# Performance work log

Hardware: AMD Instinct MI355X
Metric: run time of the kernel (lower is better)

## Reference

```python
import jax, jax.numpy as jnp
import numpy as np

B, T_ENC, FEAT, H, W2V, T_DEC, V = 32, 80, 4096, 256, 256, 30, 32000


def lstm_cell(x, h, c, w_ih, w_hh, b_ih, b_hh):
    # PyTorch LSTMCell: gates order i, f, g, o
    g = x @ w_ih.T + h @ w_hh.T + b_ih + b_hh
    i, f, gg, o = jnp.split(g, 4, axis=-1)
    c_new = jax.nn.sigmoid(f) * c + jax.nn.sigmoid(i) * jnp.tanh(gg)
    h_new = jax.nn.sigmoid(o) * jnp.tanh(c_new)
    return h_new, c_new


def setup_inputs() -> dict:
    key = jax.random.key(0)
    ks = jax.random.split(key, 13)
    s = 0.05
    return {
        'feat': jax.random.normal(ks[0], (B, T_ENC, FEAT), jnp.float32),
        'caption': jax.random.normal(ks[1], (B, T_DEC, W2V), jnp.float32),
        'caption_one_hot': jax.random.normal(ks[2], (B, T_DEC, V), jnp.float32),
        'keep_rate': 1,
        'w_ih1': jax.random.normal(ks[3], (4 * H, FEAT), jnp.float32) * s,
        'w_hh1': jax.random.normal(ks[4], (4 * H, H), jnp.float32) * s,
        'b_ih1': jax.random.normal(ks[5], (4 * H,), jnp.float32) * s,
        'b_hh1': jax.random.normal(ks[6], (4 * H,), jnp.float32) * s,
        'w_ih2': jax.random.normal(ks[7], (4 * H, H + W2V), jnp.float32) * s,
        'w_hh2': jax.random.normal(ks[8], (4 * H, H), jnp.float32) * s,
        'b_ih2': jax.random.normal(ks[9], (4 * H,), jnp.float32) * s,
        'b_hh2': jax.random.normal(ks[10], (4 * H,), jnp.float32) * s,
        'w_out': jax.random.normal(ks[11], (V, H), jnp.float32) * s,
        'b_out': jax.random.normal(ks[12], (V,), jnp.float32) * s,
    }


def reference(feat, caption, caption_one_hot, keep_rate,
              w_ih1, w_hh1, b_ih1, b_hh1,
              w_ih2, w_hh2, b_ih2, b_hh2,
              w_out, b_out):
    zeros_h = jnp.zeros((B, H), feat.dtype)
    pad1 = jnp.zeros((B, FEAT), feat.dtype)

    # ---------------- encoder: 80 steps ----------------
    def enc_step(carry, x_t):
        h1, c1, h2, c2 = carry
        h1, c1 = lstm_cell(x_t, h1, c1, w_ih1, w_hh1, b_ih1, b_hh1)
        h2, c2 = lstm_cell(jnp.concatenate([zeros_h, h1], axis=1), h2, c2,
                           w_ih2, w_hh2, b_ih2, b_hh2)
        return (h1, c1, h2, c2), h2

    (h1, c1, h2, c2), enc_h2 = jax.lax.scan(
        enc_step, (zeros_h, zeros_h, zeros_h, zeros_h),
        jnp.transpose(feat, (1, 0, 2)))
    enc_h2 = jnp.transpose(enc_h2, (1, 0, 2))  # [B, 80, H]

    # ---------------- decoder: teacher forcing (coin>=100 never fires) ----
    targets = jnp.argmax(caption_one_hot, axis=-1)  # [B, T_DEC]

    def dec_step(carry, xs):
        h1, c1, h2, c2, loss = carry
        word_t, tgt_t = xs  # [B, W2V], [B]
        h1, c1 = lstm_cell(pad1, h1, c1, w_ih1, w_hh1, b_ih1, b_hh1)
        h2n, c2 = lstm_cell(jnp.concatenate([word_t, h1], axis=1), h2, c2,
                            w_ih2, w_hh2, b_ih2, b_hh2)
        logits = h2n @ w_out.T + b_out  # [B, V]
        logp = jax.nn.log_softmax(logits, axis=-1)
        ce = -jnp.take_along_axis(logp, tgt_t[:, None], axis=1)[:, 0]
        loss = loss + jnp.mean(ce) / B  # sum(mean-CE)/batch, per original
        # attention: scores of encoder h2 states against current h2
        attn = jax.nn.softmax(jnp.einsum('bsh,bh->bs', enc_h2, h2n), axis=-1)
        ctx = jnp.einsum('bs,bsh->bh', attn, enc_h2)  # replaces h2 for next step
        return (h1, c1, ctx, c2, loss), None

    xs = (jnp.transpose(caption[:, :T_DEC - 1, :], (1, 0, 2)),
          jnp.transpose(targets[:, 1:T_DEC], (1, 0)))
    (h1, c1, h2, c2, total_loss), _ = jax.lax.scan(
        dec_step, (h1, c1, h2, c2, jnp.float32(0.0)), xs)
    return total_loss
```

## Files before the change

kernel.cpp:

```cpp
#include <hip/hip_runtime.h>
#include <hip/hip_bf16.h>
#include <math.h>

#define BB 32
#define TE 80
#define FEAT 4096
#define HH 256
#define W2V 256
#define TD 30
#define VV 32000
#define G4 1024

typedef unsigned short u16;
typedef unsigned int u32;
using f32x4 = __attribute__((ext_vector_type(4))) float;
using bf16x8 = __attribute__((ext_vector_type(8))) short;
using f16x2 = __attribute__((ext_vector_type(2))) _Float16;

#define SENT 0xFFFFFFFFu
#define GUARD (1 << 22)

__device__ __forceinline__ float sigm(float x) { return 1.0f / (1.0f + expf(-x)); }
__device__ __forceinline__ u16 f2bf(float f) {
  u32 u = __float_as_uint(f);
  u32 r = (u + 0x7FFFu + ((u >> 16) & 1u)) >> 16;
  return (u16)r;
}
__device__ __forceinline__ u32 packh2(float lo, float hi) {
  f16x2 v = {(_Float16)lo, (_Float16)hi};
  return __builtin_bit_cast(u32, v);
}

#define AT_LOAD(p)     __hip_atomic_load((p), __ATOMIC_RELAXED, __HIP_MEMORY_SCOPE_AGENT)
#define AT_STORE(p, v) __hip_atomic_store((p), (v), __ATOMIC_RELAXED, __HIP_MEMORY_SCOPE_AGENT)

__device__ __forceinline__ float fdot2h(f16x2 a, f16x2 b, float c) {
#if __has_builtin(__builtin_amdgcn_fdot2)
  return __builtin_amdgcn_fdot2(a, b, c, false);
#else
  return c + (float)a[0] * (float)b[0] + (float)a[1] * (float)b[1];
#endif
}

__global__ __launch_bounds__(256) void prep_kernel(
    const float* __restrict__ w_ih1, const float* __restrict__ w_ih2,
    const float* __restrict__ caption, const float* __restrict__ onehot,
    const float* __restrict__ b_ih1, const float* __restrict__ b_hh1,
    const float* __restrict__ b_ih2, const float* __restrict__ b_hh2,
    u16* __restrict__ w_ih1b, float* __restrict__ XW2,
    float* __restrict__ bias1, float* __restrict__ bias2,
    u32* __restrict__ H1H, u32* __restrict__ H2H, u32* __restrict__ A2P,
    float* __restrict__ loss, int* __restrict__ ctrs,
    int* __restrict__ targets) {
  __shared__ __align__(16) char psm[50688];
  int blk = blockIdx.x, tid = threadIdx.x;
  if (blk < 928) {
    int k = blk;
    int s = (k >> 5) + 1, b = k & 31;
    const float* row = &onehot[((size_t)b * TD + s) * VV];
    float bv = -INFINITY;
    int bi = 0x7fffffff;
    for (int v = tid; v < VV; v += 256) {
      float x = row[v];
      if (x > bv || (x == bv && v < bi)) { bv = x; bi = v; }
    }
    float* sv = (float*)psm;
    int* si = (int*)(psm + 1024);
    sv[tid] = bv; si[tid] = bi;
    __syncthreads();
    for (int off = 128; off; off >>= 1) {
      if (tid < off) {
        float ov = sv[tid + off]; int oi = si[tid + off];
        if (ov > sv[tid] || (ov == sv[tid] && oi < si[tid])) { sv[tid] = ov; si[tid] = oi; }
      }
      __syncthreads();
    }
    if (tid == 0) targets[k] = si[0];
  } else if (blk < 1952) {
    int i0 = (blk - 928) * 1024 + tid;
#pragma unroll
    for (int ii = 0; ii < 4; ++ii) {
      int i = i0 + ii * 256;
      float4 v = *(const float4*)&w_ih1[(size_t)i * 4];
      *(ushort4*)&w_ih1b[(size_t)i * 4] =
          make_ushort4(f2bf(v.x), f2bf(v.y), f2bf(v.z), f2bf(v.w));
    }
  } else if (blk < 2416) {
    int k = blk - 1952, nb = k & 15, t = k >> 4;
    u16* As = (u16*)psm;
    u16* Bs = (u16*)(psm + 16896);
    int nBase = nb * 64;
#pragma unroll
    for (int it = 0; it < 4; ++it) {
      int i = it * 256 + tid;
      int r = i >> 5, c8 = i & 31;
      const float* src = &caption[((size_t)r * TD + t) * 256 + c8 * 8];
      float4 v0 = *(const float4*)src;
      float4 v1 = *(const float4*)(src + 4);
      u16* dst = &As[r * 264 + c8 * 8];
      *(ushort4*)dst = make_ushort4(f2bf(v0.x), f2bf(v0.y), f2bf(v0.z), f2bf(v0.w));
      *(ushort4*)(dst + 4) = make_ushort4(f2bf(v1.x), f2bf(v1.y), f2bf(v1.z), f2bf(v1.w));
    }
#pragma unroll
    for (int it = 0; it < 8; ++it) {
      int i = it * 256 + tid;
      int r = i >> 5, c8 = i & 31;
      const float* src = &w_ih2[(size_t)(nBase + r) * 512 + c8 * 8];
      float4 v0 = *(const float4*)src;
      float4 v1 = *(const float4*)(src + 4);
      u16* dst = &Bs[r * 264 + c8 * 8];
      *(ushort4*)dst = make_ushort4(f2bf(v0.x), f2bf(v0.y), f2bf(v0.z), f2bf(v0.w));
      *(ushort4*)(dst + 4) = make_ushort4(f2bf(v1.x), f2bf(v1.y), f2bf(v1.z), f2bf(v1.w));
    }
    __syncthreads();
    int lane = tid & 63, w = tid >> 6;
    int lrow = lane & 15, lk = (lane >> 4) * 8;
    f32x4 acc[2];
    acc[0] = (f32x4){0.f, 0.f, 0.f, 0.f};
    acc[1] = (f32x4){0.f, 0.f, 0.f, 0.f};
#pragma unroll
    for (int ks = 0; ks < 8; ++ks) {
      bf16x8 bfr = *(const bf16x8*)&Bs[(w * 16 + lrow) * 264 + ks * 32 + lk];
#pragma unroll
      for (int m = 0; m < 2; ++m) {
        bf16x8 af = *(const bf16x8*)&As[(m * 16 + lrow) * 264 + ks * 32 + lk];
        acc[m] = __builtin_amdgcn_mfma_f32_16x16x32_bf16(af, bfr, acc[m], 0, 0, 0);
      }
    }
    int col = nBase + w * 16 + (lane & 15);
    float bv = b_ih2[col] + b_hh2[col];
    int orow = (lane >> 4) * 4;
#pragma unroll
    for (int m = 0; m < 2; ++m)
#pragma unroll
      for (int qq = 0; qq < 4; ++qq) {
        int bb = m * 16 + orow + qq;
        XW2[((size_t)t * 32 + bb) * G4 + col] = acc[m][qq] + bv;
      }
  } else if (blk < 2856) {
    int i = (blk - 2416) * 256 + tid;
    uint4 z = {0u, 0u, 0u, 0u};
    uint4 s = {SENT, SENT, SENT, SENT};
    uint4 v = (i < 1024) ? z : s;
    ((uint4*)H1H)[i] = v;
    ((uint4*)H2H)[i] = v;
  } else if (blk < 3296) {
    int i0 = (blk - 2856) * 1024 + tid;
    uint4 s = {SENT, SENT, SENT, SENT};
#pragma unroll
    for (int ii = 0; ii < 4; ++ii) ((uint4*)A2P)[i0 + ii * 256] = s;
  } else {
    for (int i = tid; i < 1024; i += 256) {
      bias1[i] = b_ih1[i] + b_hh1[i];
      bias2[i] = b_ih2[i] + b_hh2[i];
    }
    if (tid < 256) ctrs[tid] = 0;
    if (tid == 0) *loss = 0.0f;
  }
}

#define GBM 128
#define GBN 128
#define GBK 64
#define LDSTR 72

__global__ __launch_bounds__(256) void gemm_x1_kernel(
    const float* __restrict__ A, const u16* __restrict__ Bw,
    const float* __restrict__ bias, float* __restrict__ C) {
  __shared__ __align__(16) u16 As[GBM * LDSTR];
  __shared__ __align__(16) u16 Bs[GBN * LDSTR];
  int tid = threadIdx.x;
  int rBase = (blockIdx.x >> 3) * GBM;
  int nBase = (blockIdx.x & 7) * GBN;
  int lane = tid & 63, w = tid >> 6;
  int wrow = (w >> 1) * 64, wcol = (w & 1) * 64;
  int lrow = lane & 15, lk = (lane >> 4) * 8;

  f32x4 acc[4][4];
#pragma unroll
  for (int m = 0; m < 4; ++m)
#pragma unroll
    for (int n = 0; n < 4; ++n) acc[m][n] = (f32x4){0.f, 0.f, 0.f, 0.f};

  for (int k0 = 0; k0 < FEAT; k0 += GBK) {
#pragma unroll
    for (int i = 0; i < 8; ++i) {
      int f = i * 256 + tid;
      int r = f >> 4, c = (f & 15) << 2;
      float4 v = *(const float4*)&A[(size_t)(rBase + r) * FEAT + k0 + c];
      *(ushort4*)&As[r * LDSTR + c] =
          make_ushort4(f2bf(v.x), f2bf(v.y), f2bf(v.z), f2bf(v.w));
    }
#pragma unroll
    for (int i = 0; i < 4; ++i) {
      int f = i * 256 + tid;
      int r = f >> 3, c8 = f & 7;
      *(uint4*)&Bs[r * LDSTR + c8 * 8] =
          *(const uint4*)&Bw[(size_t)(nBase + r) * FEAT + k0 + c8 * 8];
    }
    __syncthreads();
#pragma unroll
    for (int s2 = 0; s2 < 2; ++s2) {
      bf16x8 af[4], bfr[4];
#pragma unroll
      for (int m = 0; m < 4; ++m)
        af[m] = *(const bf16x8*)&As[(wrow + m * 16 + lrow) * LDSTR + s2 * 32 + lk];
#pragma unroll
      for (int n = 0; n < 4; ++n)
        bfr[n] = *(const bf16x8*)&Bs[(wcol + n * 16 + lrow) * LDSTR + s2 * 32 + lk];
#pragma unroll
      for (int m = 0; m < 4; ++m)
#pragma unroll
        for (int n = 0; n < 4; ++n)
          acc[m][n] = __builtin_amdgcn_mfma_f32_16x16x32_bf16(
              af[m], bfr[n], acc[m][n], 0, 0, 0);
    }
    __syncthreads();
  }
  int orow = (lane >> 4) * 4;
  int ocol = lane & 15;
#pragma unroll
  for (int m = 0; m < 4; ++m)
#pragma unroll
    for (int n = 0; n < 4; ++n) {
      int cidx = nBase + wcol + n * 16 + ocol;
      float bv = bias[cidx];
#pragma unroll
      for (int q = 0; q < 4; ++q) {
        int r = rBase + wrow + m * 16 + orow + q;
        C[(size_t)r * G4 + cidx] = acc[m][n][q] + bv;
      }
    }
}

struct RP {
  const float *X1, *XW2, *bias1, *bias2;
  const float *w_hh1, *w_ih2, *w_hh2;
  u32* H1H;
  u32* H2H;
  u32* A2P;
  u16* H2NB;
};

__global__ __launch_bounds__(512, 1) void recurrent_kernel(RP p) {
  __shared__ float encL[TE][257];
  __shared__ __align__(16) f16x2 hS[128];
  __shared__ float tmp2[256];
  __shared__ float gb[256];
  __shared__ float a2pS[256];
  __shared__ float hnew[64];
  __shared__ float sc[80];
  __shared__ float red[4];
  int bid = blockIdx.x, tid = threadIdx.x;
  bool isL1 = bid < 128;
  int lb = isL1 ? bid : bid - 128;
  int b = lb >> 2, q = lb & 3;
  int r2 = tid >> 1, half = tid & 1;
  int g = r2 >> 6, jj = r2 & 63;
  int grow = (g << 8) + (q << 6) + jj;
  int jf = (q << 6) + tid;

  if (isL1) {
    f16x2 wA[64], wB[64];
    {
      const float4* sA = (const float4*)(p.w_hh1 + (size_t)grow * 256 + half * 128);
      const float4* sB = (const float4*)(p.w_ih2 + (size_t)grow * 512 + 256 + half * 128);
#pragma unroll
      for (int k = 0; k < 32; ++k) {
        float4 v = sA[k];
        wA[k * 2 + 0] = f16x2{(_Float16)v.x, (_Float16)v.y};
        wA[k * 2 + 1] = f16x2{(_Float16)v.z, (_Float16)v.w};
        float4 u = sB[k];
        wB[k * 2 + 0] = f16x2{(_Float16)u.x, (_Float16)u.y};
        wB[k * 2 + 1] = f16x2{(_Float16)u.z, (_Float16)u.w};
      }
    }
    float c1 = 0.f;
    float b1v0 = 0, b1v1 = 0, b1v2 = 0, b1v3 = 0;
    if (tid < 64) {
      b1v0 = p.bias1[jf]; b1v1 = p.bias1[256 + jf];
      b1v2 = p.bias1[512 + jf]; b1v3 = p.bias1[768 + jf];
    }
    for (int T = 0; T <= 109; ++T) {
      float x0 = b1v0, x1 = b1v1, x2 = b1v2, x3 = b1v3;
      if (tid < 64 && T < TE) {
        const float* xb = &p.X1[((size_t)b * TE + T) * G4 + jf];
        x0 = xb[0]; x1 = xb[256]; x2 = xb[512]; x3 = xb[768];
      }
      if (tid < 128) {
        const u32* src = &p.H1H[((size_t)T * 32 + b) * 128 + tid];
        u32 v = AT_LOAD(src);
        int gd = 0;
        while (v == SENT && ++gd < GUARD) {
          __builtin_amdgcn_s_sleep(1);
          v = AT_LOAD(src);
        }
        hS[tid] = __builtin_bit_cast(f16x2, v);
      }
      __syncthreads();
      float a1 = 0.f, a2 = 0.f;
      {
        const uint4* hv = ((const uint4*)hS) + half * 16;
#pragma unroll
        for (int k = 0; k < 16; ++k) {
          uint4 uu = hv[k];
          f16x2 e0 = __builtin_bit_cast(f16x2, uu.x), e1 = __builtin_bit_cast(f16x2, uu.y);
          f16x2 e2 = __builtin_bit_cast(f16x2, uu.z), e3 = __builtin_bit_cast(f16x2, uu.w);
          a1 = fdot2h(e0, wA[k * 4 + 0], a1);
          a2 = fdot2h(e0, wB[k * 4 + 0], a2);
          a1 = fdot2h(e1, wA[k * 4 + 1], a1);
          a2 = fdot2h(e1, wB[k * 4 + 1], a2);
          a1 = fdot2h(e2, wA[k * 4 + 2], a1);
          a2 = fdot2h(e2, wB[k * 4 + 2], a2);
          a1 = fdot2h(e3, wA[k * 4 + 3], a1);
          a2 = fdot2h(e3, wB[k * 4 + 3], a2);
        }
      }
      a1 += __shfl_xor(a1, 1);
      a2 += __shfl_xor(a2, 1);
      float a2o = __shfl_xor(a2, 2);
      if (half == 0) gb[r2] = a1;
      if ((tid & 3) == 0 && T >= 1) {
        int pr = tid >> 2;
        int gp = pr >> 5, wp = pr & 31;
        AT_STORE(&p.A2P[((size_t)T * 32 + b) * 512 + (gp << 7) + (q << 5) + wp],
                 packh2(a2, a2o));
      }
      __syncthreads();
      if (T <= 108) {
        if (tid < 64) {
          float gi = gb[tid] + x0;
          float gf = gb[64 + tid] + x1;
          float gG = gb[128 + tid] + x2;
          float go = gb[192 + tid] + x3;
          c1 = sigm(gf) * c1 + sigm(gi) * tanhf(gG);
          hnew[tid] = sigm(go) * tanhf(c1);
        }
        if (tid < 32) {
          u32 pk = packh2(hnew[2 * tid], hnew[2 * tid + 1]);
          AT_STORE(&p.H1H[((size_t)(T + 1) * 32 + b) * 128 + (q << 5) + tid], pk);
        }
      }
    }
  } else {
    f16x2 wC[64];
    {
      const float4* sC = (const float4*)(p.w_hh2 + (size_t)grow * 256 + half * 128);
#pragma unroll
      for (int k = 0; k < 32; ++k) {
        float4 u = sC[k];
        wC[k * 2 + 0] = f16x2{(_Float16)u.x, (_Float16)u.y};
        wC[k * 2 + 1] = f16x2{(_Float16)u.z, (_Float16)u.w};
      }
    }
    float c2 = 0.f;
    float b2v0 = 0, b2v1 = 0, b2v2 = 0, b2v3 = 0;
    if (tid < 64) {
      b2v0 = p.bias2[jf]; b2v1 = p.bias2[256 + jf];
      b2v2 = p.bias2[512 + jf]; b2v3 = p.bias2[768 + jf];
    }
    for (int U = 1; U <= 109; ++U) {
      float x0 = b2v0, x1 = b2v1, x2 = b2v2, x3 = b2v3;
      if (tid < 64 && U >= 81) {
        const float* xb = &p.XW2[((size_t)(U - 81) * 32 + b) * G4 + jf];
        x0 = xb[0]; x1 = xb[256]; x2 = xb[512]; x3 = xb[768];
      }
      if (tid < 128) {
        const u32* src = &p.H2H[((size_t)(U - 1) * 32 + b) * 128 + tid];
        u32 v = AT_LOAD(src);
        int gd = 0;
        while (v == SENT && ++gd < (GUARD << 2)) v = AT_LOAD(src);
        f16x2 hp = __builtin_bit_cast(f16x2, v);
        hS[tid] = hp;
        tmp2[2 * tid] = (float)hp[0];
        tmp2[2 * tid + 1] = (float)hp[1];
      } else if (tid < 256) {
        int rr = tid - 128;
        int gp = rr >> 5, wp = rr & 31;
        const u32* src = &p.A2P[((size_t)U * 32 + b) * 512 + (gp << 7) + (q << 5) + wp];
        u32 v = AT_LOAD(src);
        int gd = 0;
        while (v == SENT && ++gd < GUARD) {
          __builtin_amdgcn_s_sleep(1);
          v = AT_LOAD(src);
        }
        f16x2 pr = __builtin_bit_cast(f16x2, v);
        a2pS[gp * 64 + 2 * wp] = (float)pr[0];
        a2pS[gp * 64 + 2 * wp + 1] = (float)pr[1];
      }
      __syncthreads();
      float a2p0 = 0, a2p1 = 0, a2p2 = 0, a2p3 = 0;
      if (tid < 64) {
        a2p0 = a2pS[tid]; a2p1 = a2pS[64 + tid];
        a2p2 = a2pS[128 + tid]; a2p3 = a2pS[192 + tid];
      }
      if (U <= 81) {
        if (U >= 2 && tid < 256) encL[U - 2][tid] = tmp2[tid];
      } else {
        float a = 0.f;
        if (tid < TE) {
          const float* e = &encL[tid][0];
#pragma unroll 8
          for (int k2 = 0; k2 < 256; ++k2) a += e[k2] * tmp2[k2];
        }
        float av = (tid < TE) ? a : -INFINITY;
#pragma unroll
        for (int d = 32; d; d >>= 1) av = fmaxf(av, __shfl_xor(av, d));
        if (tid == 0) red[0] = av;
        if (tid == 64) red[1] = av;
        __syncthreads();
        float m = fmaxf(red[0], red[1]);
        float e2 = (tid < TE) ? expf(a - m) : 0.f;
        float sv = e2;
#pragma unroll
        for (int d = 32; d; d >>= 1) sv += __shfl_xor(sv, d);
        if (tid == 0) red[2] = sv;
        if (tid == 64) red[3] = sv;
        __syncthreads();
        float inv = 1.0f / (red[2] + red[3]);
        if (tid < TE) sc[tid] = e2 * inv;
        __syncthreads();
        if (tid < 256) {
          float acc = 0.f;
          for (int t2 = 0; t2 < TE; ++t2) acc += sc[t2] * encL[t2][tid];
          tmp2[tid] = acc;
        }
        __syncthreads();
        if (tid < 128)
          hS[tid] = f16x2{(_Float16)tmp2[2 * tid], (_Float16)tmp2[2 * tid + 1]};
      }
      __syncthreads();
      float a2 = 0.f;
      {
        const uint4* hv = ((const uint4*)hS) + half * 16;
#pragma unroll
        for (int k = 0; k < 16; ++k) {
          uint4 uu = hv[k];
          a2 = fdot2h(__builtin_bit_cast(f16x2, uu.x), wC[k * 4 + 0], a2);
          a2 = fdot2h(__builtin_bit_cast(f16x2, uu.y), wC[k * 4 + 1], a2);
          a2 = fdot2h(__builtin_bit_cast(f16x2, uu.z), wC[k * 4 + 2], a2);
          a2 = fdot2h(__builtin_bit_cast(f16x2, uu.w), wC[k * 4 + 3], a2);
        }
      }
      a2 += __shfl_xor(a2, 1);
      if (half == 0) gb[r2] = a2;
      __syncthreads();
      if (tid < 64) {
        float gi = gb[tid] + a2p0 + x0;
        float gf = gb[64 + tid] + a2p1 + x1;
        float gG = gb[128 + tid] + a2p2 + x2;
        float go = gb[192 + tid] + a2p3 + x3;
        c2 = sigm(gf) * c2 + sigm(gi) * tanhf(gG);
        float h = sigm(go) * tanhf(c2);
        hnew[tid] = h;
        if (U >= 81)
          p.H2NB[((size_t)(U - 81) * 32 + b) * 256 + jf] = f2bf(h);
      }
      if (tid < 32) {
        u32 pk = packh2(hnew[2 * tid], hnew[2 * tid + 1]);
        AT_STORE(&p.H2H[((size_t)U * 32 + b) * 128 + (q << 5) + tid], pk);
      }
    }
  }
}

__global__ __launch_bounds__(256, 1) void logits_final_kernel(
    const u16* __restrict__ H2NB, const float* __restrict__ w_out,
    const float* __restrict__ b_out, const int* __restrict__ targets,
    u32* __restrict__ pmaxA, u32* __restrict__ psumA, u32* __restrict__ tgtv,
    float* __restrict__ loss, int* __restrict__ ctrs, float* __restrict__ out) {
  __shared__ __align__(16) u16 bS[32768];
  __shared__ __align__(16) u16 aS[32 * 264];
  __shared__ int tS[32];
  __shared__ float sm[256];
  int tid = threadIdx.x, bid = blockIdx.x;
#pragma unroll
  for (int it = 0; it < 16; ++it) {
    int id = it * 256 + tid;
    int nt = id >> 9, rr = (id >> 5) & 15, kg = id & 31;
    int n = bid * 128 + nt * 16 + rr;
    const float* src = &w_out[(size_t)n * 256 + kg * 8];
    float4 v0 = *(const float4*)src;
    float4 v1 = *(const float4*)(src + 4);
    u16* dst = &bS[(size_t)((nt * 32 + kg) * 16 + rr) * 8];
    *(ushort4*)dst = make_ushort4(f2bf(v0.x), f2bf(v0.y), f2bf(v0.z), f2bf(v0.w));
    *(ushort4*)(dst + 4) = make_ushort4(f2bf(v1.x), f2bf(v1.y), f2bf(v1.z), f2bf(v1.w));
  }
  int wid = tid >> 6, lane = tid & 63, lcol = lane & 15, lk = lane >> 4;
  float bo[2];
#pragma unroll
  for (int n = 0; n < 2; ++n) bo[n] = b_out[(bid * 8 + wid * 2 + n) * 16 + lcol];

  for (int rg = 0; rg < 29; ++rg) {
    __syncthreads();
    for (int i = tid; i < 1024; i += 256) {
      int r = i >> 5, c8 = i & 31;
      *(uint4*)&aS[r * 264 + c8 * 8] =
          *(const uint4*)&H2NB[(size_t)rg * 8192 + r * 256 + c8 * 8];
    }
    if (tid < 32) tS[tid] = targets[rg * 32 + tid];
    __syncthreads();
    f32x4 acc[2][2];
#pragma unroll
    for (int m = 0; m < 2; ++m)
#pragma unroll
      for (int n = 0; n < 2; ++n) acc[m][n] = (f32x4){0.f, 0.f, 0.f, 0.f};
#pragma unroll
    for (int ks = 0; ks < 8; ++ks) {
      bf16x8 a0 = *(const bf16x8*)&aS[lcol * 264 + ks * 32 + lk * 8];
      bf16x8 a1 = *(const bf16x8*)&aS[(16 + lcol) * 264 + ks * 32 + lk * 8];
      bf16x8 b0 = *(const bf16x8*)&bS[(wid * 2) * 4096 + ((ks * 4 + lk) * 16 + lcol) * 8];
      bf16x8 b1 = *(const bf16x8*)&bS[(wid * 2 + 1) * 4096 + ((ks * 4 + lk) * 16 + lcol) * 8];
      acc[0][0] = __builtin_amdgcn_mfma_f32_16x16x32_bf16(a0, b0, acc[0][0], 0, 0, 0);
      acc[0][1] = __builtin_amdgcn_mfma_f32_16x16x32_bf16(a0, b1, acc[0][1], 0, 0, 0);
      acc[1][0] = __builtin_amdgcn_mfma_f32_16x16x32_bf16(a1, b0, acc[1][0], 0, 0, 0);
      acc[1][1] = __builtin_amdgcn_mfma_f32_16x16x32_bf16(a1, b1, acc[1][1], 0, 0, 0);
    }
    int nbase = (bid * 8 + wid * 2) * 16 + lcol;
#pragma unroll
    for (int m = 0; m < 2; ++m) {
      float pm[4], psv[4];
#pragma unroll
      for (int qq = 0; qq < 4; ++qq) {
        float v0 = acc[m][0][qq] + bo[0];
        float v1 = acc[m][1][qq] + bo[1];
        int r = m * 16 + lk * 4 + qq;
        int tg = tS[r];
        if (tg == nbase) AT_STORE(&tgtv[rg * 32 + r], __float_as_uint(v0));
        if (tg == nbase + 16) AT_STORE(&tgtv[rg * 32 + r], __float_as_uint(v1));
        float mx = fmaxf(v0, v1);
#pragma unroll
        for (int d = 1; d < 16; d <<= 1) mx = fmaxf(mx, __shfl_xor(mx, d));
        float e = expf(v0 - mx) + expf(v1 - mx);
#pragma unroll
        for (int d = 1; d < 16; d <<= 1) e += __shfl_xor(e, d);
        pm[qq] = mx;
        psv[qq] = e;
      }
      if (lcol == 0) {
        int chunk = bid * 4 + wid;
#pragma unroll
        for (int qq = 0; qq < 4; ++qq) {
          int r2 = rg * 32 + m * 16 + lk * 4 + qq;
          AT_STORE(&pmaxA[(size_t)r2 * 1000 + chunk], __float_as_uint(pm[qq]));
          AT_STORE(&psumA[(size_t)r2 * 1000 + chunk], __float_as_uint(psv[qq]));
        }
      }
    }
  }
  asm volatile("s_waitcnt vmcnt(0)" ::: "memory");
  __syncthreads();
  if (tid == 0) {
    __hip_atomic_fetch_add(&ctrs[0], 1, __ATOMIC_RELEASE, __HIP_MEMORY_SCOPE_AGENT);
    int gd = 0;
    while (__hip_atomic_load(&ctrs[0], __ATOMIC_ACQUIRE, __HIP_MEMORY_SCOPE_AGENT) < 250 &&
           ++gd < GUARD)
      __builtin_amdgcn_s_sleep(2);
  }
  __syncthreads();
#pragma unroll
  for (int k = 0; k < 4; ++k) {
    int row = bid * 4 + k;
    if (row < 928) {
      const u32* pm = pmaxA + (size_t)row * 1000;
      const u32* psv = psumA + (size_t)row * 1000;
      float m = -INFINITY;
      for (int c = tid; c < 1000; c += 256) m = fmaxf(m, __uint_as_float(AT_LOAD(&pm[c])));
      sm[tid] = m;
      __syncthreads();
      for (int off = 128; off; off >>= 1) {
        if (tid < off) sm[tid] = fmaxf(sm[tid], sm[tid + off]);
        __syncthreads();
      }
      float M = sm[0];
      __syncthreads();
      float s = 0.f;
      for (int c = tid; c < 1000; c += 256)
        s += __uint_as_float(AT_LOAD(&psv[c])) * expf(__uint_as_float(AT_LOAD(&pm[c])) - M);
      sm[tid] = s;
      __syncthreads();
      for (int off = 128; off; off >>= 1) {
        if (tid < off) sm[tid] += sm[tid + off];
        __syncthreads();
      }
      if (tid == 0) {
        float tv = __uint_as_float(AT_LOAD(&tgtv[row]));
        atomicAdd(loss, (M + logf(sm[0]) - tv) * (1.0f / 1024.0f));
      }
      __syncthreads();
    }
  }
  asm volatile("s_waitcnt vmcnt(0)" ::: "memory");
  if (tid == 0) {
    int old = __hip_atomic_fetch_add(&ctrs[32], 1, __ATOMIC_ACQ_REL, __HIP_MEMORY_SCOPE_AGENT);
    if (old == 249) out[0] = __uint_as_float(AT_LOAD((u32*)loss));
  }
}

extern "C" void kernel_launch(void* const* d_in, const int* in_sizes, int n_in,
                              void* d_out, int out_size, void* d_ws, size_t ws_size,
                              hipStream_t stream) {
  (void)in_sizes; (void)n_in; (void)out_size; (void)ws_size;
  const float* feat    = (const float*)d_in[0];
  const float* caption = (const float*)d_in[1];
  const float* onehot  = (const float*)d_in[2];
  const float* w_ih1   = (const float*)d_in[4];
  const float* w_hh1   = (const float*)d_in[5];
  const float* b_ih1   = (const float*)d_in[6];
  const float* b_hh1   = (const float*)d_in[7];
  const float* w_ih2   = (const float*)d_in[8];
  const float* w_hh2   = (const float*)d_in[9];
  const float* b_ih2   = (const float*)d_in[10];
  const float* b_hh2   = (const float*)d_in[11];
  const float* w_out   = (const float*)d_in[12];
  const float* b_out   = (const float*)d_in[13];

  char* p = (char*)d_ws;
  auto alloc = [&](size_t bytes) {
    char* r = p;
    p += (bytes + 255) & ~(size_t)255;
    return r;
  };
  float* X1      = (float*)alloc(2560ull * 1024 * 4);
  float* XW2     = (float*)alloc(29ull * 32 * 1024 * 4);
  float* bias1   = (float*)alloc(1024 * 4);
  float* bias2   = (float*)alloc(1024 * 4);
  u32*   H1H     = (u32*)alloc(110ull * 32 * 128 * 4);
  u32*   H2H     = (u32*)alloc(110ull * 32 * 128 * 4);
  u32*   A2P     = (u32*)alloc(110ull * 32 * 512 * 4);
  u16*   H2NB    = (u16*)alloc(29ull * 8192 * 2);
  u32*   pmaxA   = (u32*)alloc(928ull * 1000 * 4);
  u32*   psumA   = (u32*)alloc(928ull * 1000 * 4);
  u32*   tgtv    = (u32*)alloc(928 * 4);
  float* lossacc = (float*)alloc(256);
  int*   ctrs    = (int*)alloc(1024);
  int*   targets = (int*)alloc(29 * 32 * 4);
  u16*   w_ih1b  = (u16*)alloc(1024ull * 4096 * 2);

  prep_kernel<<<3297, 256, 0, stream>>>(
      w_ih1, w_ih2, caption, onehot,
      b_ih1, b_hh1, b_ih2, b_hh2,
      w_ih1b, XW2, bias1, bias2, H1H, H2H, A2P, lossacc, ctrs, targets);

  gemm_x1_kernel<<<160, 256, 0, stream>>>(feat, w_ih1b, bias1, X1);

  RP rp;
  rp.X1 = X1; rp.XW2 = XW2; rp.bias1 = bias1; rp.bias2 = bias2;
  rp.w_hh1 = w_hh1; rp.w_ih2 = w_ih2; rp.w_hh2 = w_hh2;
  rp.H1H = H1H; rp.H2H = H2H; rp.A2P = A2P; rp.H2NB = H2NB;
  void* args[] = {&rp};
  hipLaunchCooperativeKernel((const void*)recurrent_kernel, dim3(256), dim3(512),
                             args, 0, stream);

  logits_final_kernel<<<250, 256, 0, stream>>>(H2NB, w_out, b_out, targets,
                                               pmaxA, psumA, tgtv, lossacc, ctrs,
                                               (float*)d_out);
}
```

Baseline: 742.4 us.

## Fuse logits/CE into cooperative recurrent kernel with per-step readiness counters

Merges the separate logits/cross-entropy kernel into the persistent recurrent kernel. Blocks that finish the recurrence pull 128-column vocab chunks from an atomic work queue and process each decoder step's hidden states as soon as a per-step counter shows all 128 layer-2 blocks have published them. This overlaps the output projection with the tail of the recurrence and removes a kernel launch. The final reduction becomes a single-pass online log-sum-exp over twice as many partial chunks. The cost is that chunk-processing blocks spin-wait on step counters, and most blocks are busy in the recurrence until the end, so the overlap may be small.

```diff
diff --git a/kernel.cpp b/kernel.cpp
--- a/kernel.cpp
+++ b/kernel.cpp
@@ -30,9 +30,13 @@
   f16x2 v = {(_Float16)lo, (_Float16)hi};
   return __builtin_bit_cast(u32, v);
 }
+__device__ __forceinline__ u32 packbf2(float lo, float hi) {
+  return (u32)f2bf(lo) | ((u32)f2bf(hi) << 16);
+}
 
 #define AT_LOAD(p)     __hip_atomic_load((p), __ATOMIC_RELAXED, __HIP_MEMORY_SCOPE_AGENT)
 #define AT_STORE(p, v) __hip_atomic_store((p), (v), __ATOMIC_RELAXED, __HIP_MEMORY_SCOPE_AGENT)
+#define AT_ADD(p, v)   __hip_atomic_fetch_add((p), (v), __ATOMIC_RELAXED, __HIP_MEMORY_SCOPE_AGENT)
 
 __device__ __forceinline__ float fdot2h(f16x2 a, f16x2 b, float c) {
 #if __has_builtin(__builtin_amdgcn_fdot2)
@@ -41,6 +45,11 @@
   return c + (float)a[0] * (float)b[0] + (float)a[1] * (float)b[1];
 #endif
 }
+
+#define C_BAR 0
+#define C_WRT 32
+#define C_CHQ 96
+#define C_RG 128
 
 __global__ __launch_bounds__(256) void prep_kernel(
     const float* __restrict__ w_ih1, const float* __restrict__ w_ih2,
@@ -235,22 +244,116 @@
 
 struct RP {
   const float *X1, *XW2, *bias1, *bias2;
-  const float *w_hh1, *w_ih2, *w_hh2;
+  const float *w_hh1, *w_ih2, *w_hh2, *w_out, *b_out;
   u32* H1H;
   u32* H2H;
   u32* A2P;
-  u16* H2NB;
+  u32* H2NB32;
+  u32 *pmaxA, *psumA, *tgtv;
+  float* loss;
+  int* ctrs;
+  const int* targets;
+  float* out;
 };
 
-__global__ __launch_bounds__(512, 1) void recurrent_kernel(RP p) {
-  __shared__ float encL[TE][257];
-  __shared__ __align__(16) f16x2 hS[128];
-  __shared__ float tmp2[256];
-  __shared__ float gb[256];
-  __shared__ float a2pS[256];
-  __shared__ float hnew[64];
-  __shared__ float sc[80];
-  __shared__ float red[4];
+#define SMEMB 86528
+
+__device__ void do_logits(char* smem, const RP& p) {
+  u16* bS = (u16*)smem;
+  u16* aS = (u16*)(smem + 65536);
+  int* tS = (int*)(smem + 82432);
+  int* chS = (int*)(smem + 82560);
+  int tid = threadIdx.x;
+  int w = tid >> 6, lane = tid & 63, lcol = lane & 15, lk = lane >> 4;
+  while (true) {
+    if (tid == 0) *chS = AT_ADD(&p.ctrs[C_CHQ], 1);
+    __syncthreads();
+    int ch = *chS;
+    if (ch >= 250) break;
+#pragma unroll
+    for (int it = 0; it < 8; ++it) {
+      int id = it * 512 + tid;
+      int nt = id >> 9, rr = (id >> 5) & 15, kg = id & 31;
+      int n = ch * 128 + nt * 16 + rr;
+      const float* src = &p.w_out[(size_t)n * 256 + kg * 8];
+      float4 v0 = *(const float4*)src;
+      float4 v1 = *(const float4*)(src + 4);
+      u16* dst = &bS[(size_t)((nt * 32 + kg) * 16 + rr) * 8];
+      *(ushort4*)dst = make_ushort4(f2bf(v0.x), f2bf(v0.y), f2bf(v0.z), f2bf(v0.w));
+      *(ushort4*)(dst + 4) = make_ushort4(f2bf(v1.x), f2bf(v1.y), f2bf(v1.z), f2bf(v1.w));
+    }
+    float bo = p.b_out[ch * 128 + w * 16 + lcol];
+    for (int rg = 0; rg < 29; ++rg) {
+      if (tid == 0) {
+        int gd = 0;
+        while (AT_LOAD(&p.ctrs[C_RG + rg]) < 128 && ++gd < GUARD)
+          __builtin_amdgcn_s_sleep(1);
+      }
+      __syncthreads();
+      __builtin_amdgcn_fence(__ATOMIC_ACQUIRE, "agent");
+#pragma unroll
+      for (int it = 0; it < 2; ++it) {
+        int i = it * 512 + tid;
+        int r = i >> 5, c8 = i & 31;
+        *(uint4*)&aS[r * 264 + c8 * 8] =
+            *(const uint4*)&p.H2NB32[((size_t)rg * 32 + r) * 128 + c8 * 4];
+      }
+      if (tid < 32) tS[tid] = p.targets[rg * 32 + tid];
+      __syncthreads();
+      f32x4 acc[2];
+      acc[0] = (f32x4){0.f, 0.f, 0.f, 0.f};
+      acc[1] = (f32x4){0.f, 0.f, 0.f, 0.f};
+#pragma unroll
+      for (int ks = 0; ks < 8; ++ks) {
+        bf16x8 bfr = *(const bf16x8*)&bS[(size_t)((w * 32 + ks * 4 + lk) * 16 + lcol) * 8];
+        bf16x8 a0 = *(const bf16x8*)&aS[lcol * 264 + ks * 32 + lk * 8];
+        bf16x8 a1 = *(const bf16x8*)&aS[(16 + lcol) * 264 + ks * 32 + lk * 8];
+        acc[0] = __builtin_amdgcn_mfma_f32_16x16x32_bf16(a0, bfr, acc[0], 0, 0, 0);
+        acc[1] = __builtin_amdgcn_mfma_f32_16x16x32_bf16(a1, bfr, acc[1], 0, 0, 0);
+      }
+      int ncol = ch * 128 + w * 16 + lcol;
+      int chunkW = ch * 8 + w;
+#pragma unroll
+      for (int m = 0; m < 2; ++m) {
+        float pm[4], psv[4];
+#pragma unroll
+        for (int qq = 0; qq < 4; ++qq) {
+          float v0 = acc[m][qq] + bo;
+          int r = m * 16 + lk * 4 + qq;
+          if (tS[r] == ncol) AT_STORE(&p.tgtv[rg * 32 + r], __float_as_uint(v0));
+          float mx = v0;
+#pragma unroll
+          for (int d = 1; d < 16; d <<= 1) mx = fmaxf(mx, __shfl_xor(mx, d));
+          float e = expf(v0 - mx);
+#pragma unroll
+          for (int d = 1; d < 16; d <<= 1) e += __shfl_xor(e, d);
+          pm[qq] = mx;
+          psv[qq] = e;
+        }
+        if (lcol == 0) {
+#pragma unroll
+          for (int qq = 0; qq < 4; ++qq) {
+            int r2 = rg * 32 + m * 16 + lk * 4 + qq;
+            AT_STORE(&p.pmaxA[(size_t)r2 * 2000 + chunkW], __float_as_uint(pm[qq]));
+            AT_STORE(&p.psumA[(size_t)r2 * 2000 + chunkW], __float_as_uint(psv[qq]));
+          }
+        }
+      }
+      __syncthreads();
+    }
+  }
+}
+
+__global__ __launch_bounds__(512, 1) void mega_kernel(RP p) {
+  __shared__ __align__(16) char smem[SMEMB];
+  float* encL = (float*)smem;
+  f16x2* hS = (f16x2*)(smem + 82240);
+  float* tmp2 = (float*)(smem + 82752);
+  float* gb = (float*)(smem + 83776);
+  float* a2pS = (float*)(smem + 84800);
+  float* hnew = (float*)(smem + 85824);
+  float* sc = (float*)(smem + 86080);
+  float* red = (float*)(smem + 86400);
   int bid = blockIdx.x, tid = threadIdx.x;
   bool isL1 = bid < 128;
   int lb = isL1 ? bid : bid - 128;
@@ -395,11 +498,11 @@
         a2p2 = a2pS[128 + tid]; a2p3 = a2pS[192 + tid];
       }
       if (U <= 81) {
-        if (U >= 2 && tid < 256) encL[U - 2][tid] = tmp2[tid];
+        if (U >= 2 && tid < 256) encL[(U - 2) * 257 + tid] = tmp2[tid];
       } else {
         float a = 0.f;
         if (tid < TE) {
-          const float* e = &encL[tid][0];
+          const float* e = &encL[tid * 257];
 #pragma unroll 8
           for (int k2 = 0; k2 < 256; ++k2) a += e[k2] * tmp2[k2];
         }
@@ -422,7 +525,7 @@
         __syncthreads();
         if (tid < 256) {
           float acc = 0.f;
-          for (int t2 = 0; t2 < TE; ++t2) acc += sc[t2] * encL[t2][tid];
+          for (int t2 = 0; t2 < TE; ++t2) acc += sc[t2] * encL[t2 * 257 + tid];
           tmp2[tid] = acc;
         }
         __syncthreads();
@@ -453,147 +556,76 @@
         c2 = sigm(gf) * c2 + sigm(gi) * tanhf(gG);
         float h = sigm(go) * tanhf(c2);
         hnew[tid] = h;
-        if (U >= 81)
-          p.H2NB[((size_t)(U - 81) * 32 + b) * 256 + jf] = f2bf(h);
       }
       if (tid < 32) {
         u32 pk = packh2(hnew[2 * tid], hnew[2 * tid + 1]);
         AT_STORE(&p.H2H[((size_t)U * 32 + b) * 128 + (q << 5) + tid], pk);
+        if (U >= 81) {
+          u32 bk = packbf2(hnew[2 * tid], hnew[2 * tid + 1]);
+          AT_STORE(&p.H2NB32[((size_t)(U - 81) * 32 + b) * 128 + (q << 5) + tid], bk);
+        }
+      }
+      if (U >= 81) {
+        asm volatile("s_waitcnt vmcnt(0)" ::: "memory");
+        if (tid == 0) AT_ADD(&p.ctrs[C_RG + (U - 81)], 1);
       }
     }
   }
-}
-
-__global__ __launch_bounds__(256, 1) void logits_final_kernel(
-    const u16* __restrict__ H2NB, const float* __restrict__ w_out,
-    const float* __restrict__ b_out, const int* __restrict__ targets,
-    u32* __restrict__ pmaxA, u32* __restrict__ psumA, u32* __restrict__ tgtv,
-    float* __restrict__ loss, int* __restrict__ ctrs, float* __restrict__ out) {
-  __shared__ __align__(16) u16 bS[32768];
-  __shared__ __align__(16) u16 aS[32 * 264];
-  __shared__ int tS[32];
-  __shared__ float sm[256];
-  int tid = threadIdx.x, bid = blockIdx.x;
-#pragma unroll
-  for (int it = 0; it < 16; ++it) {
-    int id = it * 256 + tid;
-    int nt = id >> 9, rr = (id >> 5) & 15, kg = id & 31;
-    int n = bid * 128 + nt * 16 + rr;
-    const float* src = &w_out[(size_t)n * 256 + kg * 8];
-    float4 v0 = *(const float4*)src;
-    float4 v1 = *(const float4*)(src + 4);
-    u16* dst = &bS[(size_t)((nt * 32 + kg) * 16 + rr) * 8];
-    *(ushort4*)dst = make_ushort4(f2bf(v0.x), f2bf(v0.y), f2bf(v0.z), f2bf(v0.w));
-    *(ushort4*)(dst + 4) = make_ushort4(f2bf(v1.x), f2bf(v1.y), f2bf(v1.z), f2bf(v1.w));
-  }
-  int wid = tid >> 6, lane = tid & 63, lcol = lane & 15, lk = lane >> 4;
-  float bo[2];
-#pragma unroll
-  for (int n = 0; n < 2; ++n) bo[n] = b_out[(bid * 8 + wid * 2 + n) * 16 + lcol];
-
-  for (int rg = 0; rg < 29; ++rg) {
-    __syncthreads();
-    for (int i = tid; i < 1024; i += 256) {
-      int r = i >> 5, c8 = i & 31;
-      *(uint4*)&aS[r * 264 + c8 * 8] =
-          *(const uint4*)&H2NB[(size_t)rg * 8192 + r * 256 + c8 * 8];
-    }
-    if (tid < 32) tS[tid] = targets[rg * 32 + tid];
-    __syncthreads();
-    f32x4 acc[2][2];
-#pragma unroll
-    for (int m = 0; m < 2; ++m)
-#pragma unroll
-      for (int n = 0; n < 2; ++n) acc[m][n] = (f32x4){0.f, 0.f, 0.f, 0.f};
-#pragma unroll
-    for (int ks = 0; ks < 8; ++ks) {
-      bf16x8 a0 = *(const bf16x8*)&aS[lcol * 264 + ks * 32 + lk * 8];
-      bf16x8 a1 = *(const bf16x8*)&aS[(16 + lcol) * 264 + ks * 32 + lk * 8];
-      bf16x8 b0 = *(const bf16x8*)&bS[(wid * 2) * 4096 + ((ks * 4 + lk) * 16 + lcol) * 8];
-      bf16x8 b1 = *(const bf16x8*)&bS[(wid * 2 + 1) * 4096 + ((ks * 4 + lk) * 16 + lcol) * 8];
-      acc[0][0] = __builtin_amdgcn_mfma_f32_16x16x32_bf16(a0, b0, acc[0][0], 0, 0, 0);
-      acc[0][1] = __builtin_amdgcn_mfma_f32_16x16x32_bf16(a0, b1, acc[0][1], 0, 0, 0);
-      acc[1][0] = __builtin_amdgcn_mfma_f32_16x16x32_bf16(a1, b0, acc[1][0], 0, 0, 0);
-      acc[1][1] = __builtin_amdgcn_mfma_f32_16x16x32_bf16(a1, b1, acc[1][1], 0, 0, 0);
-    }
-    int nbase = (bid * 8 + wid * 2) * 16 + lcol;
-#pragma unroll
-    for (int m = 0; m < 2; ++m) {
-      float pm[4], psv[4];
-#pragma unroll
-      for (int qq = 0; qq < 4; ++qq) {
-        float v0 = acc[m][0][qq] + bo[0];
-        float v1 = acc[m][1][qq] + bo[1];
-        int r = m * 16 + lk * 4 + qq;
-        int tg = tS[r];
-        if (tg == nbase) AT_STORE(&tgtv[rg * 32 + r], __float_as_uint(v0));
-        if (tg == nbase + 16) AT_STORE(&tgtv[rg * 32 + r], __float_as_uint(v1));
-        float mx = fmaxf(v0, v1);
-#pragma unroll
-        for (int d = 1; d < 16; d <<= 1) mx = fmaxf(mx, __shfl_xor(mx, d));
-        float e = expf(v0 - mx) + expf(v1 - mx);
-#pragma unroll
-        for (int d = 1; d < 16; d <<= 1) e += __shfl_xor(e, d);
-        pm[qq] = mx;
-        psv[qq] = e;
-      }
-      if (lcol == 0) {
-        int chunk = bid * 4 + wid;
-#pragma unroll
-        for (int qq = 0; qq < 4; ++qq) {
-          int r2 = rg * 32 + m * 16 + lk * 4 + qq;
-          AT_STORE(&pmaxA[(size_t)r2 * 1000 + chunk], __float_as_uint(pm[qq]));
-          AT_STORE(&psumA[(size_t)r2 * 1000 + chunk], __float_as_uint(psv[qq]));
-        }
-      }
-    }
-  }
+  __syncthreads();
+  do_logits(smem, p);
   asm volatile("s_waitcnt vmcnt(0)" ::: "memory");
   __syncthreads();
   if (tid == 0) {
-    __hip_atomic_fetch_add(&ctrs[0], 1, __ATOMIC_RELEASE, __HIP_MEMORY_SCOPE_AGENT);
+    __hip_atomic_fetch_add(&p.ctrs[C_BAR], 1, __ATOMIC_RELEASE, __HIP_MEMORY_SCOPE_AGENT);
     int gd = 0;
-    while (__hip_atomic_load(&ctrs[0], __ATOMIC_ACQUIRE, __HIP_MEMORY_SCOPE_AGENT) < 250 &&
+    while (__hip_atomic_load(&p.ctrs[C_BAR], __ATOMIC_ACQUIRE, __HIP_MEMORY_SCOPE_AGENT) < 256 &&
            ++gd < GUARD)
       __builtin_amdgcn_s_sleep(2);
   }
   __syncthreads();
-#pragma unroll
-  for (int k = 0; k < 4; ++k) {
-    int row = bid * 4 + k;
-    if (row < 928) {
-      const u32* pm = pmaxA + (size_t)row * 1000;
-      const u32* psv = psumA + (size_t)row * 1000;
-      float m = -INFINITY;
-      for (int c = tid; c < 1000; c += 256) m = fmaxf(m, __uint_as_float(AT_LOAD(&pm[c])));
-      sm[tid] = m;
-      __syncthreads();
-      for (int off = 128; off; off >>= 1) {
-        if (tid < off) sm[tid] = fmaxf(sm[tid], sm[tid + off]);
+  __builtin_amdgcn_fence(__ATOMIC_ACQUIRE, "agent");
+  {
+    float* smM = (float*)smem;
+    float* smS = (float*)(smem + 2048);
+#pragma unroll
+    for (int k = 0; k < 4; ++k) {
+      int row = bid * 4 + k;
+      if (row < 928) {
+        const u32* pm = p.pmaxA + (size_t)row * 2000;
+        const u32* psv = p.psumA + (size_t)row * 2000;
+        float m = -INFINITY, s = 0.f;
+        for (int c = tid; c < 2000; c += 512) {
+          float pmv = __uint_as_float(pm[c]);
+          float psvv = __uint_as_float(psv[c]);
+          float mn = fmaxf(m, pmv);
+          s = s * expf(m - mn) + psvv * expf(pmv - mn);
+          m = mn;
+        }
+        smM[tid] = m;
+        smS[tid] = s;
         __syncthreads();
-      }
-      float M = sm[0];
-      __syncthreads();
-      float s = 0.f;
-      for (int c = tid; c < 1000; c += 256)
-        s += __uint_as_float(AT_LOAD(&psv[c])) * expf(__uint_as_float(AT_LOAD(&pm[c])) - M);
-      sm[tid] = s;
-      __syncthreads();
-      for (int off = 128; off; off >>= 1) {
-        if (tid < off) sm[tid] += sm[tid + off];
+        for (int off = 256; off; off >>= 1) {
+          if (tid < off) {
+            float m2 = smM[tid + off], s2 = smS[tid + off];
+            float mn = fmaxf(smM[tid], m2);
+            smS[tid] = smS[tid] * expf(smM[tid] - mn) + s2 * expf(m2 - mn);
+            smM[tid] = mn;
+          }
+          __syncthreads();
+        }
+        if (tid == 0) {
+          float tv = __uint_as_float(p.tgtv[row]);
+          atomicAdd(p.loss, (smM[0] + logf(smS[0]) - tv) * (1.0f / 1024.0f));
+        }
         __syncthreads();
       }
-      if (tid == 0) {
-        float tv = __uint_as_float(AT_LOAD(&tgtv[row]));
-        atomicAdd(loss, (M + logf(sm[0]) - tv) * (1.0f / 1024.0f));
-      }
-      __syncthreads();
     }
   }
   asm volatile("s_waitcnt vmcnt(0)" ::: "memory");
   if (tid == 0) {
-    int old = __hip_atomic_fetch_add(&ctrs[32], 1, __ATOMIC_ACQ_REL, __HIP_MEMORY_SCOPE_AGENT);
-    if (old == 249) out[0] = __uint_as_float(AT_LOAD((u32*)loss));
+    int old = __hip_atomic_fetch_add(&p.ctrs[C_WRT], 1, __ATOMIC_ACQ_REL,
+                                     __HIP_MEMORY_SCOPE_AGENT);
+    if (old == 255) p.out[0] = __uint_as_float(AT_LOAD((u32*)p.loss));
   }
 }
 
@@ -628,9 +660,9 @@
   u32*   H1H     = (u32*)alloc(110ull * 32 * 128 * 4);
   u32*   H2H     = (u32*)alloc(110ull * 32 * 128 * 4);
   u32*   A2P     = (u32*)alloc(110ull * 32 * 512 * 4);
-  u16*   H2NB    = (u16*)alloc(29ull * 8192 * 2);
-  u32*   pmaxA   = (u32*)alloc(928ull * 1000 * 4);
-  u32*   psumA   = (u32*)alloc(928ull * 1000 * 4);
+  u32*   H2NB32  = (u32*)alloc(29ull * 32 * 128 * 4);
+  u32*   pmaxA   = (u32*)alloc(928ull * 2000 * 4);
+  u32*   psumA   = (u32*)alloc(928ull * 2000 * 4);
   u32*   tgtv    = (u32*)alloc(928 * 4);
   float* lossacc = (float*)alloc(256);
   int*   ctrs    = (int*)alloc(1024);
@@ -647,12 +679,12 @@
   RP rp;
   rp.X1 = X1; rp.XW2 = XW2; rp.bias1 = bias1; rp.bias2 = bias2;
   rp.w_hh1 = w_hh1; rp.w_ih2 = w_ih2; rp.w_hh2 = w_hh2;
-  rp.H1H = H1H; rp.H2H = H2H; rp.A2P = A2P; rp.H2NB = H2NB;
+  rp.w_out = w_out; rp.b_out = b_out;
+  rp.H1H = H1H; rp.H2H = H2H; rp.A2P = A2P; rp.H2NB32 = H2NB32;
+  rp.pmaxA = pmaxA; rp.psumA = psumA; rp.tgtv = tgtv;
+  rp.loss = lossacc; rp.ctrs = ctrs; rp.targets = targets;
+  rp.out = (float*)d_out;
   void* args[] = {&rp};
-  hipLaunchCooperativeKernel((const void*)recurrent_kernel, dim3(256), dim3(512),
+  hipLaunchCooperativeKernel((const void*)mega_kernel, dim3(256), dim3(512),
                              args, 0, stream);
-
-  logits_final_kernel<<<250, 256, 0, stream>>>(H2NB, w_out, b_out, targets,
-                                               pmaxA, psumA, tgtv, lossacc, ctrs,
-                                               (float*)d_out);
-}
+}
```

Result: slower. 1.211 ms (+63.1%).
